# Kernel tuning notes

Measured on AMD Instinct MI355X. Metric: run time of the kernel, lower is better.

## Reference

```python
import jax, jax.numpy as jnp
import numpy as np

MAX_VIEWS = 50   # n_view in _hard_anchor_sampling
IGNORE = 255
TEMP = 0.07


def _sample_indices(labels, predict, max_classes, n_view, rng):
    # Faithful numpy port of _hard_anchor_sampling's index selection
    # (hard = predicted-as-c but mislabeled, easy = correct), host-side since
    # the torch original is data-dependent (nonzero/randperm per class).
    B, N = labels.shape
    idx = np.zeros((B, max_classes, n_view), dtype=np.int64)
    half = n_view // 2
    for b in range(B):
        yh, y = labels[b], predict[b]
        cls = [c for c in np.unique(yh) if c != IGNORE and (yh == c).sum() > n_view]
        for n, c in enumerate(cls[:max_classes]):
            hard = np.where((yh == c) & (y != c))[0]
            easy = np.where((yh == c) & (y == c))[0]
            nh_, ne_ = len(hard), len(easy)
            if nh_ >= half and ne_ >= half:
                nh, ne = half, n_view - half
            elif nh_ >= half:
                ne = ne_; nh = n_view - ne
            else:
                nh = nh_; ne = n_view - nh
            sel = np.concatenate([rng.permutation(hard)[:nh], rng.permutation(easy)[:ne]])
            idx[b, n] = sel
        # with uniform random labels over 19 classes and 16384 pixels, every
        # class qualifies, so the 'fill remaining slots' branch never triggers.
    return idx


def setup_inputs() -> dict:
    B, C, H, W = 4, 256, 128, 128
    NC = 19
    key = jax.random.key(0)
    k1, k2 = jax.random.split(key)
    feats_q = jax.random.normal(k1, (B, C, H, W), dtype=jnp.float32)
    feats_k = jax.random.normal(k2, (B, C, H, W), dtype=jnp.float32)
    rng = np.random.default_rng(0)
    labels = rng.integers(0, NC, size=(B, H * W))
    predict = rng.integers(0, NC, size=(B, H * W))
    sample_idx = jnp.asarray(_sample_indices(labels, predict, NC, MAX_VIEWS, rng))
    return {"feats_q": feats_q, "feats_k": feats_k, "sample_idx": sample_idx}


def _neg_cols(nc, nv):
    # static column indices surviving the ~diag_block boolean mask (row-major)
    P = nc * nv
    cols = np.arange(P)
    return np.stack([cols[(cols // nv) != (i // nv)] for i in range(P)])  # [P, P-nv]


def _forward(feats_q, feats_k, sample_idx):
    B, C, H, W = feats_q.shape
    _, nc, nv = sample_idx.shape
    P = nc * nv
    q = feats_q.transpose(0, 2, 3, 1).reshape(B, H * W, C)
    k = jax.lax.stop_gradient(feats_k).transpose(0, 2, 3, 1).reshape(B, H * W, C)  # detach
    bidx = jnp.arange(B)[:, None, None]
    Xq = q[bidx, sample_idx]  # [B, nc, nv, C] gathered anchors
    Xk = k[bidx, sample_idx]
    # positives: per-patch q.k
    l_pos = jnp.einsum('bnvc,bnvc->bnv', Xq, Xk).reshape(-1, 1)  # [B*P, 1]
    # negatives: full within-batch similarity, minus same-class diagonal blocks
    qf = Xq.reshape(B, P, C)
    kf = Xk.reshape(B, P, C)
    sim = jnp.einsum('bpc,bqc->bpq', qf, kf)  # [B, P, P]
    neg_cols = jnp.asarray(_neg_cols(nc, nv))  # [P, P-nv]
    l_neg = jnp.take_along_axis(sim, neg_cols[None], axis=2).reshape(B * P, P - nv)
    out = jnp.concatenate([l_pos, l_neg], axis=1) / TEMP
    # CrossEntropyLoss(reduction='none') with target 0
    return -jax.nn.log_softmax(out, axis=1)[:, 0]  # [B*P]


def reference(feats_q, feats_k, sample_idx):
    return _forward(feats_q, feats_k, sample_idx)
```

## Files before the change

kernel.cpp:

```cpp
#include <hip/hip_runtime.h>
#include <math.h>

#define BB 4
#define CC 256
#define HW (128*128)
#define NC 19
#define NV 50
#define PP 950
#define INV_T (1.0f/0.07f)
#define PLANE ((size_t)BB * PP * CC)
#define NCG 8
#define LDSP 40
#define NCHK 64
#define MAXE 64

typedef short bf16x8 __attribute__((ext_vector_type(8)));
typedef float f32x4  __attribute__((ext_vector_type(4)));

static __device__ __forceinline__ unsigned short f2bf(float f) {
    unsigned int u = __float_as_uint(f);
    unsigned int r = (u + 0x7fffu + ((u >> 16) & 1u)) >> 16;
    return (unsigned short)r;
}
static __device__ __forceinline__ float bf2f(unsigned short h) {
    return __uint_as_float(((unsigned int)h) << 16);
}
__device__ __forceinline__ void lse_merge(float& m, float& s, float m2, float s2) {
    float nm = fmaxf(m, m2);
    float e1 = __expf(m - nm);
    float e2 = __expf(m2 - nm);
    s = s * e1 + s2 * e2;
    m = nm;
}

__global__ __launch_bounds__(1024)
void mapbuild_kernel(const int* __restrict__ sidx,
                     int* __restrict__ clist, int* __restrict__ ccnt) {
    __shared__ int lcnt[NCHK];
    __shared__ int lent[NCHK * MAXE];
    int b = blockIdx.x;
    int tid = threadIdx.x;
    if (tid < NCHK) lcnt[tid] = 0;
    __syncthreads();
    if (tid < PP) {
        int pix = sidx[b * PP + tid];
        int chunk = pix >> 8, pl = pix & 255;
        int pos = atomicAdd(&lcnt[chunk], 1);
        if (pos < MAXE) lent[chunk * MAXE + pos] = (tid << 8) | pl;
    }
    __syncthreads();
    if (tid < NCHK) {
        int c = lcnt[tid];
        ccnt[b * NCHK + tid] = c < MAXE ? c : MAXE;
    }
    for (int i = tid; i < NCHK * MAXE; i += 1024)
        clist[b * NCHK * MAXE + i] = lent[i];
}

__global__ __launch_bounds__(256)
void gather_kernel(const float* __restrict__ fq, const float* __restrict__ fk,
                   const int* __restrict__ clist, const int* __restrict__ ccnt,
                   unsigned short* __restrict__ xqh, unsigned short* __restrict__ xql,
                   unsigned short* __restrict__ xkh, unsigned short* __restrict__ xkl) {
    __shared__ short pxmap[256];
    __shared__ short slotarr[MAXE];
    __shared__ short bufh[MAXE][32];
    __shared__ short bufl[MAXE][32];

    int x = blockIdx.x;
    int chunk  = x & 63;
    int tensor = (x >> 6) & 1;
    int b      = (x >> 7) & 3;
    int cg     = x >> 9;
    int px0 = chunk * 256;

    int tid = threadIdx.x;
    int cnt = ccnt[b * NCHK + chunk];

    pxmap[tid] = -1;
    __syncthreads();
    if (tid < cnt) {
        int e = clist[(b * NCHK + chunk) * MAXE + tid];
        slotarr[tid] = (short)(e >> 8);
        pxmap[e & 255] = (short)tid;
    }
    __syncthreads();

    const float* f = tensor ? fk : fq;
    unsigned short* oh = tensor ? xkh : xqh;
    unsigned short* ol = tensor ? xkl : xql;

    int lp  = tid & 15;
    int chl = tid >> 4;
    int ch0 = cg * 32 + chl;
    int ch1 = ch0 + 16;
    const float* s0 = f + ((size_t)b * CC + ch0) * HW + px0;
    const float* s1 = f + ((size_t)b * CC + ch1) * HW + px0;

    float4 v[8];
#pragma unroll
    for (int i = 0; i < 4; ++i) v[i]     = *(const float4*)(s0 + (i * 16 + lp) * 4);
#pragma unroll
    for (int i = 0; i < 4; ++i) v[4 + i] = *(const float4*)(s1 + (i * 16 + lp) * 4);

#pragma unroll
    for (int k = 0; k < 8; ++k) {
        int i = k & 3;
        int lch = (k < 4) ? chl : (chl + 16);
#pragma unroll
        for (int e = 0; e < 4; ++e) {
            int px = i * 64 + lp * 4 + e;
            int le = pxmap[px];
            if (le >= 0) {
                float val = ((const float*)&v[k])[e];
                unsigned short h = f2bf(val);
                bufh[le][lch] = (short)h;
                bufl[le][lch] = (short)f2bf(val - bf2f(h));
            }
        }
    }
    __syncthreads();

#pragma unroll
    for (int rep = 0; rep < 2; ++rep) {
        int e = rep * 32 + (tid >> 3);
        int plane = (tid >> 2) & 1, q = tid & 3;
        if (e < cnt) {
            int slot = slotarr[e];
            size_t dst = ((size_t)b * PP + slot) * CC + cg * 32 + q * 8;
            const short* sp = (plane ? &bufl[e][0] : &bufh[e][0]) + q * 8;
            *(int4*)((plane ? ol : oh) + dst) = *(const int4*)sp;
        }
    }
}

#define MF(ACC, AF, BF) ACC = __builtin_amdgcn_mfma_f32_16x16x32_bf16(AF, BF, ACC, 0, 0, 0)

#define STEP(KT) do {                                                           \
    int4 rh_, rl_;                                                              \
    if ((KT) < 7) {                                                             \
        rh_ = *(const int4*)(xkh + stage_src + ((KT) + 1) * 32);                \
        rl_ = *(const int4*)(xkl + stage_src + ((KT) + 1) * 32);                \
    }                                                                           \
    const short* bbase_ = &bl[(KT) & 1][0][0] + lr * LDSP + lg * 8;             \
    _Pragma("unroll")                                                           \
    for (int ct = 0; ct < 8; ++ct) {                                            \
        const short* bp_ = bbase_ + ct * (16 * LDSP);                           \
        bf16x8 Bh_ = *(const bf16x8*)bp_;                                       \
        bf16x8 Bl_ = *(const bf16x8*)(bp_ + 128 * LDSP);                        \
        MF(acc[ct], Ah[KT], Bh_);                                               \
        MF(acc[ct], Al[KT], Bh_);                                               \
        MF(acc[ct], Ah[KT], Bl_);                                               \
    }                                                                           \
    if ((KT) < 7) {                                                             \
        *(int4*)&bl[((KT) + 1) & 1][0][stage_dst] = rh_;                        \
        *(int4*)&bl[((KT) + 1) & 1][1][stage_dst] = rl_;                        \
        __syncthreads();                                                        \
    }                                                                           \
} while (0)

__global__ __launch_bounds__(512)
void nce_mfma(const unsigned short* __restrict__ xqh, const unsigned short* __restrict__ xql,
              const unsigned short* __restrict__ xkh, const unsigned short* __restrict__ xkl,
              float* __restrict__ pos, float* __restrict__ pm, float* __restrict__ ps) {
    __shared__ short bl[2][2][128 * LDSP];

    int cg = blockIdx.x;
    int rb = blockIdx.y;
    int b  = blockIdx.z;
    int tid = threadIdx.x;
    int w = tid >> 6, l = tid & 63;
    int lr = l & 15, lg = l >> 4;

    int uc = tid >> 2, uq = tid & 3;
    int gcol = cg * 128 + uc; if (gcol > PP - 1) gcol = PP - 1;
    size_t stage_src = ((size_t)b * PP + gcol) * CC + uq * 8;
    int stage_dst = uc * LDSP + uq * 8;

    int arow = rb * 128 + w * 16 + lr; if (arow > PP - 1) arow = PP - 1;
    size_t abase = ((size_t)b * PP + arow) * CC + lg * 8;
    bf16x8 Ah[8], Al[8];
#pragma unroll
    for (int kt = 0; kt < 8; ++kt) {
        Ah[kt] = *(const bf16x8*)(xqh + abase + kt * 32);
        Al[kt] = *(const bf16x8*)(xql + abase + kt * 32);
    }

    {
        int4 rh = *(const int4*)(xkh + stage_src);
        int4 rl = *(const int4*)(xkl + stage_src);
        *(int4*)&bl[0][0][stage_dst] = rh;
        *(int4*)&bl[0][1][stage_dst] = rl;
    }
    __syncthreads();

    f32x4 acc[8];
#pragma unroll
    for (int ct = 0; ct < 8; ++ct) acc[ct] = (f32x4){0.f, 0.f, 0.f, 0.f};

    STEP(0); STEP(1); STEP(2); STEP(3);
    STEP(4); STEP(5); STEP(6); STEP(7);

#pragma unroll
    for (int j = 0; j < 4; ++j) {
        int row = rb * 128 + w * 16 + lg * 4 + j;
        bool rowok = row < PP;
        int rcls = row / NV;
        float m = -1e30f, s = 0.f;
#pragma unroll
        for (int ct = 0; ct < 8; ++ct) {
            int col = cg * 128 + ct * 16 + lr;
            bool colok = col < PP;
            int ccls = col / NV;
            float x = acc[ct][j] * INV_T;
            bool ok = rowok && colok && ((ccls != rcls) || (col == row));
            if (rowok && col == row) pos[(size_t)b * 960 + row] = x;
            float xm = ok ? x : -1e30f;
            float nm = fmaxf(m, xm);
            float e1 = __expf(m - nm);
            float e2 = ok ? __expf(x - nm) : 0.f;
            s = s * e1 + e2; m = nm;
        }
#pragma unroll
        for (int off = 1; off <= 8; off <<= 1) {
            float m2 = __shfl_xor(m, off, 64);
            float s2 = __shfl_xor(s, off, 64);
            lse_merge(m, s, m2, s2);
        }
        if (lr == 0 && rowok) {
            pm[((size_t)b * NCG + cg) * 960 + row] = m;
            ps[((size_t)b * NCG + cg) * 960 + row] = s;
        }
    }
}

__global__ __launch_bounds__(256)
void finalize_kernel(const float* __restrict__ pm, const float* __restrict__ ps,
                     const float* __restrict__ pos, float* __restrict__ out) {
    int i = blockIdx.x * 256 + threadIdx.x;
    if (i >= BB * PP) return;
    int b = i / PP, row = i - b * PP;
    float m = -1e30f, s = 0.f;
#pragma unroll
    for (int g = 0; g < NCG; ++g) {
        size_t o = ((size_t)b * NCG + g) * 960 + row;
        lse_merge(m, s, pm[o], ps[o]);
    }
    out[i] = m + logf(s) - pos[(size_t)b * 960 + row];
}

extern "C" void kernel_launch(void* const* d_in, const int* in_sizes, int n_in,
                              void* d_out, int out_size, void* d_ws, size_t ws_size,
                              hipStream_t stream) {
    const float* fq   = (const float*)d_in[0];
    const float* fk   = (const float*)d_in[1];
    const int*   sidx = (const int*)d_in[2];
    float* outp = (float*)d_out;

    char* p = (char*)d_ws;
    unsigned short* xqh = (unsigned short*)p; p += PLANE * 2;
    unsigned short* xql = (unsigned short*)p; p += PLANE * 2;
    unsigned short* xkh = (unsigned short*)p; p += PLANE * 2;
    unsigned short* xkl = (unsigned short*)p; p += PLANE * 2;
    int*          clist = (int*)p;            p += (size_t)BB * NCHK * MAXE * 4;
    int*           ccnt = (int*)p;            p += (size_t)BB * NCHK * 4;
    float*          pos = (float*)p;          p += (size_t)BB * 960 * 4;
    float*           pm = (float*)p;          p += (size_t)BB * NCG * 960 * 4;
    float*           ps = (float*)p;

    mapbuild_kernel<<<dim3(BB), 1024, 0, stream>>>(sidx, clist, ccnt);
    gather_kernel<<<dim3(4096), 256, 0, stream>>>(fq, fk, clist, ccnt, xqh, xql, xkh, xkl);
    nce_mfma<<<dim3(NCG, 8, BB), 512, 0, stream>>>(xqh, xql, xkh, xkl, pos, pm, ps);
    finalize_kernel<<<dim3((BB * PP + 255) / 256), 256, 0, stream>>>(pm, ps, pos, outp);
}
```

Measured before the change: 51.47 us.

## Enlarge gather chunks to 1024 pixels with double-buffered register loads

The gather kernel now handles 1024-pixel super-chunks instead of 256-pixel chunks, so it launches a quarter as many blocks. Each block walks four 256-pixel sub-chunks and alternates two register buffers, issuing the next global load before processing the current one to overlap memory latency with the bf16 split. The pixel map lookups are vectorised, and the per-chunk entry cap rises to 128 with larger LDS buffers. Costs are higher register and LDS use per block and fewer blocks available to spread across CUs. If more than 128 sampled pixels fall in one super-chunk, the extras are dropped.

New measurement: 52.73 us. 1.02x slower.

```diff
diff --git a/kernel.cpp b/kernel.cpp
--- a/kernel.cpp
+++ b/kernel.cpp
@@ -11,11 +11,12 @@
 #define PLANE ((size_t)BB * PP * CC)
 #define NCG 8
 #define LDSP 40
-#define NCHK 64
-#define MAXE 64
+#define NSC 16
+#define MAXE 128
 
 typedef short bf16x8 __attribute__((ext_vector_type(8)));
 typedef float f32x4  __attribute__((ext_vector_type(4)));
+typedef short short4v __attribute__((ext_vector_type(4)));
 
 static __device__ __forceinline__ unsigned short f2bf(float f) {
     unsigned int u = __float_as_uint(f);
@@ -36,53 +37,83 @@
 __global__ __launch_bounds__(1024)
 void mapbuild_kernel(const int* __restrict__ sidx,
                      int* __restrict__ clist, int* __restrict__ ccnt) {
-    __shared__ int lcnt[NCHK];
-    __shared__ int lent[NCHK * MAXE];
+    __shared__ int lcnt[NSC];
+    __shared__ int lent[NSC * MAXE];
     int b = blockIdx.x;
     int tid = threadIdx.x;
-    if (tid < NCHK) lcnt[tid] = 0;
+    if (tid < NSC) lcnt[tid] = 0;
     __syncthreads();
     if (tid < PP) {
         int pix = sidx[b * PP + tid];
-        int chunk = pix >> 8, pl = pix & 255;
-        int pos = atomicAdd(&lcnt[chunk], 1);
-        if (pos < MAXE) lent[chunk * MAXE + pos] = (tid << 8) | pl;
-    }
-    __syncthreads();
-    if (tid < NCHK) {
+        int sc = pix >> 10, pl = pix & 1023;
+        int pos = atomicAdd(&lcnt[sc], 1);
+        if (pos < MAXE) lent[sc * MAXE + pos] = (tid << 10) | pl;
+    }
+    __syncthreads();
+    if (tid < NSC) {
         int c = lcnt[tid];
-        ccnt[b * NCHK + tid] = c < MAXE ? c : MAXE;
-    }
-    for (int i = tid; i < NCHK * MAXE; i += 1024)
-        clist[b * NCHK * MAXE + i] = lent[i];
-}
+        ccnt[b * NSC + tid] = c < MAXE ? c : MAXE;
+    }
+    for (int i = tid; i < NSC * MAXE; i += 1024)
+        clist[b * NSC * MAXE + i] = lent[i];
+}
+
+#define GLOAD(BUF, C) do {                                                      \
+    _Pragma("unroll")                                                           \
+    for (int i = 0; i < 4; ++i) {                                               \
+        BUF[i]     = *(const float4*)(s0 + (C) * 256 + i * 64);                 \
+        BUF[4 + i] = *(const float4*)(s1 + (C) * 256 + i * 64);                 \
+    }                                                                           \
+} while (0)
+
+#define GPROC(BUF, C) do {                                                      \
+    _Pragma("unroll")                                                           \
+    for (int half = 0; half < 2; ++half) {                                      \
+        int lch = chl + half * 16;                                              \
+        _Pragma("unroll")                                                       \
+        for (int i = 0; i < 4; ++i) {                                           \
+            int pxl = (C) * 256 + i * 64 + lp * 4;                              \
+            short4v mp = *(const short4v*)&pxmap[pxl];                          \
+            float4 v = BUF[half * 4 + i];                                       \
+            _Pragma("unroll")                                                   \
+            for (int e = 0; e < 4; ++e) {                                       \
+                int le = mp[e];                                                 \
+                if (le >= 0) {                                                  \
+                    float val = ((const float*)&v)[e];                          \
+                    unsigned short h = f2bf(val);                               \
+                    bufh[le][lch] = (short)h;                                   \
+                    bufl[le][lch] = (short)f2bf(val - bf2f(h));                 \
+                }                                                               \
+            }                                                                   \
+        }                                                                       \
+    }                                                                           \
+} while (0)
 
 __global__ __launch_bounds__(256)
 void gather_kernel(const float* __restrict__ fq, const float* __restrict__ fk,
                    const int* __restrict__ clist, const int* __restrict__ ccnt,
                    unsigned short* __restrict__ xqh, unsigned short* __restrict__ xql,
                    unsigned short* __restrict__ xkh, unsigned short* __restrict__ xkl) {
-    __shared__ short pxmap[256];
+    __shared__ short pxmap[1024];
     __shared__ short slotarr[MAXE];
     __shared__ short bufh[MAXE][32];
     __shared__ short bufl[MAXE][32];
 
     int x = blockIdx.x;
-    int chunk  = x & 63;
-    int tensor = (x >> 6) & 1;
-    int b      = (x >> 7) & 3;
-    int cg     = x >> 9;
-    int px0 = chunk * 256;
+    int cg     = x & 7;
+    int sc     = (x >> 3) & 15;
+    int tensor = (x >> 7) & 1;
+    int b      = x >> 8;
 
     int tid = threadIdx.x;
-    int cnt = ccnt[b * NCHK + chunk];
-
-    pxmap[tid] = -1;
+    int cnt = ccnt[b * NSC + sc];
+
+    if (tid < 128) ((int4*)pxmap)[tid] = make_int4(-1, -1, -1, -1);
     __syncthreads();
     if (tid < cnt) {
-        int e = clist[(b * NCHK + chunk) * MAXE + tid];
-        slotarr[tid] = (short)(e >> 8);
-        pxmap[e & 255] = (short)tid;
+        int e = clist[(b * NSC + sc) * MAXE + tid];
+        slotarr[tid] = (short)(e >> 10);
+        pxmap[e & 1023] = (short)tid;
     }
     __syncthreads();
 
@@ -90,45 +121,26 @@
     unsigned short* oh = tensor ? xkh : xqh;
     unsigned short* ol = tensor ? xkl : xql;
 
-    int lp  = tid & 15;
-    int chl = tid >> 4;
-    int ch0 = cg * 32 + chl;
-    int ch1 = ch0 + 16;
-    const float* s0 = f + ((size_t)b * CC + ch0) * HW + px0;
-    const float* s1 = f + ((size_t)b * CC + ch1) * HW + px0;
-
-    float4 v[8];
-#pragma unroll
-    for (int i = 0; i < 4; ++i) v[i]     = *(const float4*)(s0 + (i * 16 + lp) * 4);
-#pragma unroll
-    for (int i = 0; i < 4; ++i) v[4 + i] = *(const float4*)(s1 + (i * 16 + lp) * 4);
-
-#pragma unroll
-    for (int k = 0; k < 8; ++k) {
-        int i = k & 3;
-        int lch = (k < 4) ? chl : (chl + 16);
-#pragma unroll
-        for (int e = 0; e < 4; ++e) {
-            int px = i * 64 + lp * 4 + e;
-            int le = pxmap[px];
-            if (le >= 0) {
-                float val = ((const float*)&v[k])[e];
-                unsigned short h = f2bf(val);
-                bufh[le][lch] = (short)h;
-                bufl[le][lch] = (short)f2bf(val - bf2f(h));
-            }
-        }
-    }
-    __syncthreads();
-
-#pragma unroll
-    for (int rep = 0; rep < 2; ++rep) {
-        int e = rep * 32 + (tid >> 3);
+    int lp = tid & 15, chl = tid >> 4;
+    int ch0 = cg * 32 + chl, ch1 = ch0 + 16;
+    const float* s0 = f + ((size_t)b * CC + ch0) * HW + sc * 1024 + lp * 4;
+    const float* s1 = f + ((size_t)b * CC + ch1) * HW + sc * 1024 + lp * 4;
+
+    float4 va[8], vb[8];
+    GLOAD(va, 0); GLOAD(vb, 1);
+    GPROC(va, 0); GLOAD(va, 2);
+    GPROC(vb, 1); GLOAD(vb, 3);
+    GPROC(va, 2); GPROC(vb, 3);
+    __syncthreads();
+
+#pragma unroll
+    for (int r = 0; r < 4; ++r) {
+        int entry = r * 32 + (tid >> 3);
         int plane = (tid >> 2) & 1, q = tid & 3;
-        if (e < cnt) {
-            int slot = slotarr[e];
+        if (entry < cnt) {
+            int slot = slotarr[entry];
             size_t dst = ((size_t)b * PP + slot) * CC + cg * 32 + q * 8;
-            const short* sp = (plane ? &bufl[e][0] : &bufh[e][0]) + q * 8;
+            const short* sp = (plane ? &bufl[entry][0] : &bufh[entry][0]) + q * 8;
             *(int4*)((plane ? ol : oh) + dst) = *(const int4*)sp;
         }
     }
@@ -262,14 +274,14 @@
     unsigned short* xql = (unsigned short*)p; p += PLANE * 2;
     unsigned short* xkh = (unsigned short*)p; p += PLANE * 2;
     unsigned short* xkl = (unsigned short*)p; p += PLANE * 2;
-    int*          clist = (int*)p;            p += (size_t)BB * NCHK * MAXE * 4;
-    int*           ccnt = (int*)p;            p += (size_t)BB * NCHK * 4;
+    int*          clist = (int*)p;            p += (size_t)BB * NSC * MAXE * 4;
+    int*           ccnt = (int*)p;            p += (size_t)BB * NSC * 4;
     float*          pos = (float*)p;          p += (size_t)BB * 960 * 4;
     float*           pm = (float*)p;          p += (size_t)BB * NCG * 960 * 4;
     float*           ps = (float*)p;
 
     mapbuild_kernel<<<dim3(BB), 1024, 0, stream>>>(sidx, clist, ccnt);
-    gather_kernel<<<dim3(4096), 256, 0, stream>>>(fq, fk, clist, ccnt, xqh, xql, xkh, xkl);
+    gather_kernel<<<dim3(1024), 256, 0, stream>>>(fq, fk, clist, ccnt, xqh, xql, xkh, xkl);
     nce_mfma<<<dim3(NCG, 8, BB), 512, 0, stream>>>(xqh, xql, xkh, xkl, pos, pm, ps);
     finalize_kernel<<<dim3((BB * PP + 255) / 256), 256, 0, stream>>>(pm, ps, pos, outp);
 }
```
